# Performance work log

Measured on AMD Instinct MI355X. Metric: run time of the kernel, lower is better.

The kernel has to match this reference:

```python
import jax, jax.numpy as jnp
import numpy as np

N_NODES = 50000
N_EDGES = 800000
IN_CH = 128
HID_CH = 128


def setup_inputs() -> dict:
    key = jax.random.key(0)
    k1, k2, k3, k4 = jax.random.split(key, 4)
    x = jax.random.normal(k1, (N_NODES, IN_CH), dtype=jnp.float32)
    edge_index = jax.random.randint(k2, (2, N_EDGES), 0, N_NODES, dtype=jnp.int32)
    # Glorot-ish init for weights
    W1 = jax.random.normal(k3, (IN_CH, HID_CH), dtype=jnp.float32) / np.sqrt(IN_CH)
    b1 = jnp.zeros((HID_CH,), dtype=jnp.float32)
    W2 = jax.random.normal(k4, (HID_CH, 1), dtype=jnp.float32) / np.sqrt(HID_CH)
    b2 = jnp.zeros((1,), dtype=jnp.float32)
    return {"x": x, "edge_index": edge_index, "W1": W1, "b1": b1, "W2": W2, "b2": b2}


def gcn_conv(x, W, b, src, dst, n_nodes):
    """PyG GCNConv: add self-loops, symmetric deg normalization, linear + bias."""
    h = x @ W  # [N, out]
    # degree including self-loop (edge weights are 1)
    deg = jnp.zeros((n_nodes,), dtype=h.dtype).at[dst].add(1.0) + 1.0
    dinv = jax.lax.rsqrt(deg)  # deg >= 1, safe
    norm = dinv[src] * dinv[dst]  # [E]
    msg = h[src] * norm[:, None]  # gather + edgewise scale
    out = jax.ops.segment_sum(msg, dst, num_segments=n_nodes)
    # self-loop contribution: norm_ii = dinv[i]^2
    out = out + h * (dinv * dinv)[:, None]
    return out + b


def reference(x, edge_index, W1, b1, W2, b2):
    src, dst = edge_index[0], edge_index[1]
    n = x.shape[0]
    z = jax.nn.relu(gcn_conv(x, W1, b1, src, dst, n))
    z = gcn_conv(z, W2, b2, src, dst, n)  # [N, 1]
    # decode: edgewise dot product + sigmoid
    logits = jnp.sum(z[src] * z[dst], axis=1)  # [E]
    return jax.nn.sigmoid(logits)
```

## Files before the change

kernel.cpp:

```cpp
#include <hip/hip_runtime.h>
#include <hip/hip_bf16.h>
#include <math.h>

#define N_NODES 50000
#define N_EDGES 800000
#define CH 128
#define WID 64
#define PADN 50000
#define SH 8
#define NBKT 196
#define BCAP 5120

typedef _Float16 half4t __attribute__((ext_vector_type(4)));
typedef _Float16 half8t __attribute__((ext_vector_type(8)));
typedef float    floatx4 __attribute__((ext_vector_type(4)));

__global__ void k_pre(int* __restrict__ gcur, const float* __restrict__ W,
                      _Float16* __restrict__ Whg,
                      const float* __restrict__ b1, const float* __restrict__ W2,
                      float* __restrict__ b1p, float* __restrict__ W2p) {
    const int b = blockIdx.x, t = threadIdx.x;
    if (b == 0) {
        gcur[t] = 0;
        if (t < 128) {
            int c = (t & 7) * 16 + (t >> 3);
            b1p[t] = b1[c];
            W2p[t] = W2[c];
        }
    } else {
        int o = ((b - 1) * 256 + t) * 4;
        int kg = o >> 9;
        int n  = (o >> 2) & 127;
        half4t v;
#pragma unroll
        for (int e = 0; e < 4; ++e) v[e] = (_Float16)W[(kg * 4 + e) * 128 + n];
        *(half4t*)(Whg + o) = v;
    }
}

__global__ __launch_bounds__(256) void k_bin(const int* __restrict__ src,
                                             const int* __restrict__ dst,
                                             int* __restrict__ gcur,
                                             unsigned int* __restrict__ pairs, int E) {
    __shared__ int hist[NBKT];
    __shared__ int gpos[NBKT];
    const int t = threadIdx.x;
    if (t < NBKT) hist[t] = 0;
    __syncthreads();
    const int e0 = blockIdx.x * 2048 + t * 8;
    int bb[8], rr[8];
    unsigned int vv[8];
    if (e0 + 7 < E) {
        int4 s4a = *(const int4*)(src + e0);
        int4 s4b = *(const int4*)(src + e0 + 4);
        int4 d4a = *(const int4*)(dst + e0);
        int4 d4b = *(const int4*)(dst + e0 + 4);
        int ss[8] = {s4a.x, s4a.y, s4a.z, s4a.w, s4b.x, s4b.y, s4b.z, s4b.w};
        int dd[8] = {d4a.x, d4a.y, d4a.z, d4a.w, d4b.x, d4b.y, d4b.z, d4b.w};
#pragma unroll
        for (int i = 0; i < 8; ++i) {
            bb[i] = dd[i] >> SH;
            vv[i] = (unsigned int)ss[i] | ((unsigned int)(dd[i] & 255) << 16);
            rr[i] = atomicAdd(&hist[bb[i]], 1);
        }
    } else {
#pragma unroll
        for (int i = 0; i < 8; ++i) {
            int e = e0 + i;
            bb[i] = -1;
            if (e < E) {
                int d = dst[e];
                bb[i] = d >> SH;
                vv[i] = (unsigned int)src[e] | ((unsigned int)(d & 255) << 16);
                rr[i] = atomicAdd(&hist[bb[i]], 1);
            }
        }
    }
    __syncthreads();
    if (t < NBKT) {
        int c = hist[t];
        gpos[t] = (c > 0) ? atomicAdd(&gcur[t], c) : 0;
    }
    __syncthreads();
#pragma unroll
    for (int i = 0; i < 8; ++i) {
        if (bb[i] >= 0) {
            int p = gpos[bb[i]] + rr[i];
            if (p < BCAP) pairs[(size_t)bb[i] * BCAP + p] = vv[i];
        }
    }
}

__global__ __launch_bounds__(256) void k_build(const int* __restrict__ gcur,
                                               const unsigned int* __restrict__ pairs,
                                               unsigned short* __restrict__ ell,
                                               int* __restrict__ cnt_g,
                                               float* __restrict__ dinv,
                                               _Float16* __restrict__ hs, int N) {
    __shared__ unsigned short ell_s[256 * WID];
    __shared__ int cnt_s[256];
    const int t = threadIdx.x, b = blockIdx.x;
    cnt_s[t] = 0;
    {
        unsigned int* lw = (unsigned int*)ell_s;
#pragma unroll
        for (int i = 0; i < 32; ++i) lw[t + 256 * i] = 0xC350C350u;
    }
    __syncthreads();
    const int cntb = min(gcur[b], BCAP);
    const unsigned int* pp = pairs + (size_t)b * BCAP;
    for (int j = t; j < cntb; j += 256) {
        unsigned int u = pp[j];
        int lo = u >> 16;
        int c = atomicAdd(&cnt_s[lo], 1);
        if (c < WID) ell_s[lo * WID + c] = (unsigned short)(u & 0xFFFFu);
    }
    __syncthreads();
    const unsigned int* ls = (const unsigned int*)ell_s;
    unsigned int* lg = (unsigned int*)ell + (size_t)b * (256 * WID / 2);
#pragma unroll
    for (int i = 0; i < 32; ++i) lg[t + 256 * i] = ls[t + 256 * i];
    int node = b * 256 + t;
    if (node < N) {
        cnt_g[node] = cnt_s[t];
        dinv[node]  = rsqrtf((float)cnt_s[t] + 1.0f);
    }
    if (b == 0 && t < 64)
        ((float*)(hs + (size_t)PADN * CH))[t] = 0.f;
}

__global__ __launch_bounds__(256) void k_gemm(const float* __restrict__ x,
                                              const _Float16* __restrict__ Whg,
                                              const float* __restrict__ dinv,
                                              _Float16* __restrict__ hs, int M) {
    __shared__ _Float16 Wh[32 * 128 * 4];
    const int tid = threadIdx.x;
    {
        const uint4* wg = (const uint4*)Whg;
        uint4* wl = (uint4*)Wh;
#pragma unroll
        for (int i = 0; i < 8; ++i) wl[tid + 256 * i] = wg[tid + 256 * i];
    }
    __syncthreads();

    const int w    = tid >> 6;
    const int lane = tid & 63;
    const int lrow = lane & 15;
    const int lhi  = lane >> 4;
    const int r0   = blockIdx.x * 128 + w * 16 + lrow;
    const int r1   = r0 + 64;
    const bool v0  = r0 < M;
    const bool v1  = r1 < M;
    const float* xp0 = x + (size_t)r0 * CH;
    const float* xp1 = x + (size_t)r1 * CH;

    floatx4 acc0[8], acc1[8];
#pragma unroll
    for (int t = 0; t < 8; ++t) {
        acc0[t] = (floatx4){0.f, 0.f, 0.f, 0.f};
        acc1[t] = (floatx4){0.f, 0.f, 0.f, 0.f};
    }

#pragma unroll
    for (int s = 0; s < 8; ++s) {
        floatx4 xa0 = (floatx4){0.f, 0.f, 0.f, 0.f};
        floatx4 xa1 = (floatx4){0.f, 0.f, 0.f, 0.f};
        if (v0) xa0 = *(const floatx4*)(xp0 + s * 16 + lhi * 4);
        if (v1) xa1 = *(const floatx4*)(xp1 + s * 16 + lhi * 4);
        half4t a0, a1;
#pragma unroll
        for (int e = 0; e < 4; ++e) { a0[e] = (_Float16)xa0[e]; a1[e] = (_Float16)xa1[e]; }
        const int kg = s * 4 + lhi;
#pragma unroll
        for (int t = 0; t < 8; ++t) {
            half4t bv = *(const half4t*)&Wh[(kg * 128 + t * 16 + lrow) * 4];
            acc0[t] = __builtin_amdgcn_mfma_f32_16x16x16f16(a0, bv, acc0[t], 0, 0, 0);
            acc1[t] = __builtin_amdgcn_mfma_f32_16x16x16f16(a1, bv, acc1[t], 0, 0, 0);
        }
    }

    const int base0 = blockIdx.x * 128 + w * 16 + lhi * 4;
    const int base1 = base0 + 64;
    if (base0 < M) {
        floatx4 dv = *(const floatx4*)(dinv + base0);
#pragma unroll
        for (int i = 0; i < 4; ++i) {
            half8t o;
#pragma unroll
            for (int t = 0; t < 8; ++t) o[t] = (_Float16)(acc0[t][i] * dv[i]);
            *(half8t*)(hs + (size_t)(base0 + i) * CH + lrow * 8) = o;
        }
    }
    if (base1 < M) {
        floatx4 dv = *(const floatx4*)(dinv + base1);
#pragma unroll
        for (int i = 0; i < 4; ++i) {
            half8t o;
#pragma unroll
            for (int t = 0; t < 8; ++t) o[t] = (_Float16)(acc1[t][i] * dv[i]);
            *(half8t*)(hs + (size_t)(base1 + i) * CH + lrow * 8) = o;
        }
    }
}

__global__ __launch_bounds__(256) void k_agg1(const _Float16* __restrict__ hs,
                                              const float* __restrict__ dinv,
                                              const float* __restrict__ b1p,
                                              const float* __restrict__ W2p,
                                              const int* __restrict__ cnt,
                                              const unsigned short* __restrict__ ell,
                                              float* __restrict__ h2s, int N) {
    const int w     = threadIdx.x >> 6;
    const int lane  = threadIdx.x & 63;
    const int h     = lane >> 5;
    const int hl    = lane & 31;
    const int l     = hl & 15;
    const int sub   = hl >> 4;
    const int shft  = sub << 4;
    const int hbase = h << 5;

    int node = (blockIdx.x * 4 + w) * 2 + h;
    if (node >= N) return;
    int deg = min(cnt[node], WID);
    int idxP = ((const int*)ell)[(size_t)node * (WID / 2) + hl];
    half8t self = *(const half8t*)(hs + (size_t)node * CH + 8 * l);

    float accf[8];
    if (sub == 0) {
#pragma unroll
        for (int c = 0; c < 8; ++c) accf[c] = (float)self[c];
    } else {
#pragma unroll
        for (int c = 0; c < 8; ++c) accf[c] = 0.f;
    }

    int k = 0;
    for (int j0 = sub; j0 < deg; j0 += 8, ++k) {
        int p = 4 * k;
        int w0 = __shfl(idxP, hbase | p);
        int w1 = __shfl(idxP, hbase | (p + 1));
        int w2 = __shfl(idxP, hbase | (p + 2));
        int w3 = __shfl(idxP, hbase | (p + 3));
        int s0 = (w0 >> shft) & 0xFFFF;
        int s1 = (w1 >> shft) & 0xFFFF;
        int s2 = (w2 >> shft) & 0xFFFF;
        int s3 = (w3 >> shft) & 0xFFFF;
        half8t v0 = *(const half8t*)(hs + (size_t)s0 * CH + 8 * l);
        half8t v1 = *(const half8t*)(hs + (size_t)s1 * CH + 8 * l);
        half8t v2 = *(const half8t*)(hs + (size_t)s2 * CH + 8 * l);
        half8t v3 = *(const half8t*)(hs + (size_t)s3 * CH + 8 * l);
        half8t s01 = v0 + v1;
        half8t s23 = v2 + v3;
        half8t sS  = s01 + s23;
#pragma unroll
        for (int c = 0; c < 8; ++c) accf[c] += (float)sS[c];
    }
#pragma unroll
    for (int c = 0; c < 8; ++c) accf[c] += __shfl_xor(accf[c], 16);

    float di = dinv[node];
    floatx4 bv0 = *(const floatx4*)(b1p + 8 * l);
    floatx4 bv1 = *(const floatx4*)(b1p + 8 * l + 4);
    floatx4 wv0 = *(const floatx4*)(W2p + 8 * l);
    floatx4 wv1 = *(const floatx4*)(W2p + 8 * l + 4);
    float a = 0.f;
#pragma unroll
    for (int c = 0; c < 4; ++c) {
        a += fmaxf(fmaf(accf[c], di, bv0[c]), 0.f) * wv0[c];
        a += fmaxf(fmaf(accf[c + 4], di, bv1[c]), 0.f) * wv1[c];
    }
    a += __shfl_down(a, 8);
    a += __shfl_down(a, 4);
    a += __shfl_down(a, 2);
    a += __shfl_down(a, 1);
    if (hl == 0) h2s[node] = a * di;
}

__global__ __launch_bounds__(256) void k_agg2(const float* __restrict__ h2s,
                                              const float* __restrict__ dinv,
                                              const float* __restrict__ b2,
                                              const int* __restrict__ cnt,
                                              const unsigned short* __restrict__ ell,
                                              float* __restrict__ out2, int N) {
    int t = blockIdx.x * blockDim.x + threadIdx.x;
    int node = t >> 3;
    int gl = t & 7;
    if (node >= N) return;
    int deg = min(cnt[node], WID);
    float acc = 0.f;
    for (int j = gl; j < deg; j += 8)
        acc += h2s[ell[(size_t)node * WID + j]];
    acc += __shfl_xor(acc, 4);
    acc += __shfl_xor(acc, 2);
    acc += __shfl_xor(acc, 1);
    if (gl == 0) out2[node] = fmaf(acc + h2s[node], dinv[node], b2[0]);
}

__global__ void k_decode(const float* __restrict__ out2, const int* __restrict__ src,
                         const int* __restrict__ dst, float* __restrict__ out, int E) {
    int t = blockIdx.x * blockDim.x + threadIdx.x;
    int e0 = t * 4;
    if (e0 + 3 < E) {
        int4 s4 = *(const int4*)(src + e0);
        int4 d4 = *(const int4*)(dst + e0);
        float4 o;
        o.x = 1.0f / (1.0f + __expf(-out2[s4.x] * out2[d4.x]));
        o.y = 1.0f / (1.0f + __expf(-out2[s4.y] * out2[d4.y]));
        o.z = 1.0f / (1.0f + __expf(-out2[s4.z] * out2[d4.z]));
        o.w = 1.0f / (1.0f + __expf(-out2[s4.w] * out2[d4.w]));
        *(float4*)(out + e0) = o;
    } else {
        for (int e = e0; e < E; ++e) {
            float z = out2[src[e]] * out2[dst[e]];
            out[e] = 1.0f / (1.0f + __expf(-z));
        }
    }
}

extern "C" void kernel_launch(void* const* d_in, const int* in_sizes, int n_in,
                              void* d_out, int out_size, void* d_ws, size_t ws_size,
                              hipStream_t stream) {
    const float* x   = (const float*)d_in[0];
    const int*   ei  = (const int*)d_in[1];
    const float* W1  = (const float*)d_in[2];
    const float* b1  = (const float*)d_in[3];
    const float* W2  = (const float*)d_in[4];
    const float* b2  = (const float*)d_in[5];
    float* out = (float*)d_out;

    const int N = N_NODES;
    const int E = N_EDGES;
    const int* src = ei;
    const int* dst = ei + E;

    const int NP = 50176;
    float* ws    = (float*)d_ws;
    float* dinv  = ws;
    int*   cnt   = (int*)(ws + NP);
    float* h2s   = ws + 2 * NP;
    float* out2  = ws + 3 * NP;
    float* b1p   = ws + 4 * NP;
    float* W2p   = b1p + CH;
    _Float16* Whg = (_Float16*)(W2p + CH);
    int*   gcur  = (int*)(W2p + CH + 8192);
    unsigned int* pairs = (unsigned int*)(gcur + 256);
    unsigned short* ell = (unsigned short*)(pairs + (size_t)NBKT * BCAP);
    _Float16* hs = (_Float16*)((unsigned int*)ell + (size_t)NP * WID / 2);

    k_pre<<<17, 256, 0, stream>>>(gcur, W1, Whg, b1, W2, b1p, W2p);

    k_bin<<<(E + 2047) / 2048, 256, 0, stream>>>(src, dst, gcur, pairs, E);
    k_build<<<NBKT, 256, 0, stream>>>(gcur, pairs, ell, cnt, dinv, hs, N);

    k_gemm<<<(N + 127) / 128, 256, 0, stream>>>(x, Whg, dinv, hs, N);

    k_agg1<<<(N + 7) / 8, 256, 0, stream>>>(hs, dinv, b1p, W2p, cnt, ell, h2s, N);
    k_agg2<<<(N * 8 + 255) / 256, 256, 0, stream>>>(h2s, dinv, b2, cnt, ell, out2, N);
    k_decode<<<(E / 4 + 255) / 256, 256, 0, stream>>>(out2, src, dst, out, E);
}
```

Measured before the change: 82.77 us.

## Map four nodes per wavefront in layer-1 aggregation and use fast reciprocal in decode

The layer-1 aggregation kernel now gives each node 16 lanes instead of 32, so a wavefront serves four nodes. Each lane gathers all neighbours for its 8 channels, which removes the cross-half shuffle reduction. The loop runs to the maximum degree among the four nodes, relying on padded ELL entries pointing at a zero row, and padded nodes get zero count and unit dinv so no out-of-range guard is needed. The change cuts idle lanes and launch width for low-degree nodes, at the cost of lanes waiting on the largest degree in the group. The decode sigmoid also switches to the hardware approximate reciprocal, which slightly reduces precision.

Measured after the change: 83.71 us. No clear change (+1.1%).

```diff
diff --git a/kernel.cpp b/kernel.cpp
--- a/kernel.cpp
+++ b/kernel.cpp
@@ -124,6 +124,9 @@
     if (node < N) {
         cnt_g[node] = cnt_s[t];
         dinv[node]  = rsqrtf((float)cnt_s[t] + 1.0f);
+    } else {
+        cnt_g[node] = 0;
+        dinv[node]  = 1.0f;
     }
     if (b == 0 && t < 64)
         ((float*)(hs + (size_t)PADN * CH))[t] = 0.f;
@@ -212,57 +215,63 @@
                                               float* __restrict__ h2s, int N) {
     const int w     = threadIdx.x >> 6;
     const int lane  = threadIdx.x & 63;
-    const int h     = lane >> 5;
-    const int hl    = lane & 31;
-    const int l     = hl & 15;
-    const int sub   = hl >> 4;
-    const int shft  = sub << 4;
-    const int hbase = h << 5;
-
-    int node = (blockIdx.x * 4 + w) * 2 + h;
-    if (node >= N) return;
-    int deg = min(cnt[node], WID);
-    int idxP = ((const int*)ell)[(size_t)node * (WID / 2) + hl];
-    half8t self = *(const half8t*)(hs + (size_t)node * CH + 8 * l);
+    const int q     = lane >> 4;
+    const int ql    = lane & 15;
+    const int qb    = lane & 48;
+
+    const int node = blockIdx.x * 16 + w * 4 + q;
+    const int deg  = min(cnt[node], WID);
+    const int* ellp = (const int*)ell + (size_t)node * (WID / 2);
+    int idxP  = ellp[ql];
+    int idxP2 = ellp[16 + ql];
+    half8t self = *(const half8t*)(hs + (size_t)node * CH + 8 * ql);
+
+    int dm = deg;
+    dm = max(dm, __shfl_xor(dm, 16));
+    dm = max(dm, __shfl_xor(dm, 32));
 
     float accf[8];
-    if (sub == 0) {
-#pragma unroll
-        for (int c = 0; c < 8; ++c) accf[c] = (float)self[c];
-    } else {
-#pragma unroll
-        for (int c = 0; c < 8; ++c) accf[c] = 0.f;
-    }
-
-    int k = 0;
-    for (int j0 = sub; j0 < deg; j0 += 8, ++k) {
-        int p = 4 * k;
-        int w0 = __shfl(idxP, hbase | p);
-        int w1 = __shfl(idxP, hbase | (p + 1));
-        int w2 = __shfl(idxP, hbase | (p + 2));
-        int w3 = __shfl(idxP, hbase | (p + 3));
-        int s0 = (w0 >> shft) & 0xFFFF;
-        int s1 = (w1 >> shft) & 0xFFFF;
-        int s2 = (w2 >> shft) & 0xFFFF;
-        int s3 = (w3 >> shft) & 0xFFFF;
-        half8t v0 = *(const half8t*)(hs + (size_t)s0 * CH + 8 * l);
-        half8t v1 = *(const half8t*)(hs + (size_t)s1 * CH + 8 * l);
-        half8t v2 = *(const half8t*)(hs + (size_t)s2 * CH + 8 * l);
-        half8t v3 = *(const half8t*)(hs + (size_t)s3 * CH + 8 * l);
-        half8t s01 = v0 + v1;
-        half8t s23 = v2 + v3;
-        half8t sS  = s01 + s23;
+#pragma unroll
+    for (int c = 0; c < 8; ++c) accf[c] = (float)self[c];
+
+    for (int j0 = 0, lim = min(dm, 32); j0 < lim; j0 += 4) {
+        int p  = j0 >> 1;
+        int wA = __shfl(idxP, qb | p);
+        int wB = __shfl(idxP, qb | (p + 1));
+        int s0 = wA & 0xFFFF;
+        int s1 = (wA >> 16) & 0xFFFF;
+        int s2 = wB & 0xFFFF;
+        int s3 = (wB >> 16) & 0xFFFF;
+        half8t v0 = *(const half8t*)(hs + (size_t)s0 * CH + 8 * ql);
+        half8t v1 = *(const half8t*)(hs + (size_t)s1 * CH + 8 * ql);
+        half8t v2 = *(const half8t*)(hs + (size_t)s2 * CH + 8 * ql);
+        half8t v3 = *(const half8t*)(hs + (size_t)s3 * CH + 8 * ql);
+        half8t sS = (v0 + v1) + (v2 + v3);
 #pragma unroll
         for (int c = 0; c < 8; ++c) accf[c] += (float)sS[c];
     }
-#pragma unroll
-    for (int c = 0; c < 8; ++c) accf[c] += __shfl_xor(accf[c], 16);
+    for (int j0 = 32; j0 < dm; j0 += 4) {
+        int p  = (j0 - 32) >> 1;
+        int wA = __shfl(idxP2, qb | p);
+        int wB = __shfl(idxP2, qb | (p + 1));
+        int s0 = wA & 0xFFFF;
+        int s1 = (wA >> 16) & 0xFFFF;
+        int s2 = wB & 0xFFFF;
+        int s3 = (wB >> 16) & 0xFFFF;
+        half8t v0 = *(const half8t*)(hs + (size_t)s0 * CH + 8 * ql);
+        half8t v1 = *(const half8t*)(hs + (size_t)s1 * CH + 8 * ql);
+        half8t v2 = *(const half8t*)(hs + (size_t)s2 * CH + 8 * ql);
+        half8t v3 = *(const half8t*)(hs + (size_t)s3 * CH + 8 * ql);
+        half8t sS = (v0 + v1) + (v2 + v3);
+#pragma unroll
+        for (int c = 0; c < 8; ++c) accf[c] += (float)sS[c];
+    }
 
     float di = dinv[node];
-    floatx4 bv0 = *(const floatx4*)(b1p + 8 * l);
-    floatx4 bv1 = *(const floatx4*)(b1p + 8 * l + 4);
-    floatx4 wv0 = *(const floatx4*)(W2p + 8 * l);
-    floatx4 wv1 = *(const floatx4*)(W2p + 8 * l + 4);
+    floatx4 bv0 = *(const floatx4*)(b1p + 8 * ql);
+    floatx4 bv1 = *(const floatx4*)(b1p + 8 * ql + 4);
+    floatx4 wv0 = *(const floatx4*)(W2p + 8 * ql);
+    floatx4 wv1 = *(const floatx4*)(W2p + 8 * ql + 4);
     float a = 0.f;
 #pragma unroll
     for (int c = 0; c < 4; ++c) {
@@ -273,7 +282,7 @@
     a += __shfl_down(a, 4);
     a += __shfl_down(a, 2);
     a += __shfl_down(a, 1);
-    if (hl == 0) h2s[node] = a * di;
+    if (ql == 0 && node < N) h2s[node] = a * di;
 }
 
 __global__ __launch_bounds__(256) void k_agg2(const float* __restrict__ h2s,
@@ -304,15 +313,15 @@
         int4 s4 = *(const int4*)(src + e0);
         int4 d4 = *(const int4*)(dst + e0);
         float4 o;
-        o.x = 1.0f / (1.0f + __expf(-out2[s4.x] * out2[d4.x]));
-        o.y = 1.0f / (1.0f + __expf(-out2[s4.y] * out2[d4.y]));
-        o.z = 1.0f / (1.0f + __expf(-out2[s4.z] * out2[d4.z]));
-        o.w = 1.0f / (1.0f + __expf(-out2[s4.w] * out2[d4.w]));
+        o.x = __builtin_amdgcn_rcpf(1.0f + __expf(-out2[s4.x] * out2[d4.x]));
+        o.y = __builtin_amdgcn_rcpf(1.0f + __expf(-out2[s4.y] * out2[d4.y]));
+        o.z = __builtin_amdgcn_rcpf(1.0f + __expf(-out2[s4.z] * out2[d4.z]));
+        o.w = __builtin_amdgcn_rcpf(1.0f + __expf(-out2[s4.w] * out2[d4.w]));
         *(float4*)(out + e0) = o;
     } else {
         for (int e = e0; e < E; ++e) {
             float z = out2[src[e]] * out2[dst[e]];
-            out[e] = 1.0f / (1.0f + __expf(-z));
+            out[e] = __builtin_amdgcn_rcpf(1.0f + __expf(-z));
         }
     }
 }
@@ -354,7 +363,7 @@
 
     k_gemm<<<(N + 127) / 128, 256, 0, stream>>>(x, Whg, dinv, hs, N);
 
-    k_agg1<<<(N + 7) / 8, 256, 0, stream>>>(hs, dinv, b1p, W2p, cnt, ell, h2s, N);
+    k_agg1<<<(N + 15) / 16, 256, 0, stream>>>(hs, dinv, b1p, W2p, cnt, ell, h2s, N);
     k_agg2<<<(N * 8 + 255) / 256, 256, 0, stream>>>(h2s, dinv, b2, cnt, ell, out2, N);
     k_decode<<<(E / 4 + 255) / 256, 256, 0, stream>>>(out2, src, dst, out, E);
 }
```
